# Kernel optimization log

Hardware: AMD Instinct MI355X
Metric: run time of the kernel (lower is better)

The kernel has to match this reference:

```python
import jax, jax.numpy as jnp
import numpy as np

N_TOKENS = 16384
MODEL_DIM = 2048
NUM_EXPERTS = 16
TOP_K = 2
CAPACITY_FACTOR = 1.0
NUM_SPLIT = 2  # os.environ 'num_split' default in source


def setup_inputs() -> dict:
    key = jax.random.key(0)
    kx, kw = jax.random.split(key)
    x = jax.random.normal(kx, (N_TOKENS, MODEL_DIM), dtype=jnp.float32)
    # kaiming_normal_ on Linear weight: std = sqrt(2 / fan_in)
    wg = jax.random.normal(kw, (NUM_EXPERTS, MODEL_DIM), dtype=jnp.float32) * np.float32(np.sqrt(2.0 / MODEL_DIM))
    return {"x": x, "wg": wg}


def _loss_compute(logits):
    gates = jax.nn.softmax(logits, axis=1)              # [N, E]
    num_experts = logits.shape[1]
    indices1_s = jnp.argmax(gates, axis=1)              # [N]
    mask1 = jax.nn.one_hot(indices1_s, num_experts, dtype=gates.dtype)
    me = jnp.mean(gates, axis=0)
    ce = jnp.mean(mask1, axis=0)
    l_aux = jnp.sum(me * ce) * num_experts
    return l_aux, indices1_s, gates


def _dispatch_fix_capacity(gates, k, capacity_factor, num_split):
    # gates is detached in the original (torch .detach())
    gates = jax.lax.stop_gradient(gates)
    n, e = gates.shape
    capacity = int(k * n // e * capacity_factor) // num_split * num_split
    values, topk_idx = jax.lax.top_k(gates, k)          # [N, k]
    weights = values
    flat_experts = topk_idx.reshape(-1)                 # [N*k]
    order = jnp.argsort(flat_experts)                   # stable sort by expert id
    experts_sorted = flat_experts[order]
    token_ids = jnp.repeat(jnp.arange(n, dtype=jnp.int32), k)[order]
    # position of each routed token within its expert's run
    counts = jax.ops.segment_sum(jnp.ones_like(flat_experts, dtype=jnp.int32), flat_experts, num_segments=e)
    starts = jnp.cumsum(counts) - counts                # exclusive prefix sum
    pos = jnp.arange(n * k, dtype=jnp.int32) - starts[experts_sorted]
    # fixed-capacity index table, -1 = empty slot; overflow tokens dropped
    ind = jnp.full((e, capacity), -1, dtype=jnp.int32)
    ind = ind.at[experts_sorted, pos].set(token_ids, mode="drop")  # pos>=capacity dropped
    indices = ind.reshape(-1)                           # [E*capacity], expert-major
    mask = indices >= 0
    expert_ids = jnp.repeat(jnp.arange(e, dtype=gates.dtype), capacity)
    return weights, indices, expert_ids, mask


def reference(x, wg):
    logits = jnp.einsum("nd,ed->ne", x, wg)             # Linear, no bias
    l_aux, _indices1, gates = _loss_compute(logits)
    weights, indices, expert_ids, mask = _dispatch_fix_capacity(
        gates, TOP_K, CAPACITY_FACTOR, NUM_SPLIT)
    return l_aux, weights, indices, expert_ids
```

## Files before the change

kernel.cpp:

```cpp
#include <hip/hip_runtime.h>
#include <hip/hip_bf16.h>
#include <stdint.h>

#define N_TOKENS    16384
#define MODEL_DIM   2048
#define NUM_EXPERTS 16
#define CAPACITY    2048
#define NBLK2       512
#define NBLK        256
#define GBLK        512
#define W_OFF       1
#define IDX_OFF     (1 + 2 * N_TOKENS)
#define EID_OFF     (IDX_OFF + NUM_EXPERTS * CAPACITY)

#define SC_E01    0
#define SC_CNTH   16384
#define SC_CEH    32768
#define SC_ME     49152

#define DPPX(v, ctrl) __int_as_float(__builtin_amdgcn_update_dpp(             \
    0, __float_as_int(v), (ctrl), 0xF, 0xF, true))
#define SWZ(v, off) __int_as_float(__builtin_amdgcn_ds_swizzle(               \
    __float_as_int(v), (off)))

__global__ __launch_bounds__(512) void k_logits(
    const float* __restrict__ x, const float* __restrict__ wg,
    float* __restrict__ out, uint8_t* __restrict__ ws)
{
  __shared__ float part[8][32][2][17];
  const int tid = threadIdx.x;
  const int b = blockIdx.x;
  const int l = tid & 63;
  const int kr = tid >> 6;
  const int kb = kr * 256 + l * 4;
  const int rot = l & 15;

  float4 w[16];
#pragma unroll
  for (int i = 0; i < NUM_EXPERTS; ++i)
    w[i] = *reinterpret_cast<const float4*>(wg + (size_t)((i ^ rot) * MODEL_DIM) + kb);

  const float* xp = x + (size_t)(b * 32) * MODEL_DIM + kb;

  float4 xc[4];
#pragma unroll
  for (int i = 0; i < 4; ++i)
    xc[i] = *reinterpret_cast<const float4*>(xp + (size_t)i * MODEL_DIM);

  for (int tb = 0; tb < 8; ++tb) {
    float4 xn[4];
    if (tb < 7) {
#pragma unroll
      for (int i = 0; i < 4; ++i)
        xn[i] = *reinterpret_cast<const float4*>(
            xp + (size_t)(tb * 4 + 4 + i) * MODEL_DIM);
    }
#pragma unroll
    for (int i = 0; i < 4; ++i) {
      const int t = tb * 4 + i;
      float cur[16];
#pragma unroll
      for (int j = 0; j < NUM_EXPERTS; ++j)
        cur[j] = xc[i].x * w[j].x + xc[i].y * w[j].y +
                 xc[i].z * w[j].z + xc[i].w * w[j].w;

#pragma unroll
      for (int r = 0; r < 8; ++r) cur[r] = cur[2 * r] + DPPX(cur[2 * r + 1], 0xB1);
#pragma unroll
      for (int r = 0; r < 4; ++r) cur[r] = cur[2 * r] + DPPX(cur[2 * r + 1], 0x4E);
#pragma unroll
      for (int r = 0; r < 2; ++r) cur[r] = cur[2 * r] + SWZ(cur[2 * r + 1], 0x101F);
      float v = cur[0] + DPPX(cur[1], 0x128);
      v += SWZ(v, 0x401F);
      if ((l & 31) < 16) part[kr][t][l >> 5][l & 15] = v;
    }
#pragma unroll
    for (int i = 0; i < 4; ++i) xc[i] = xn[i];
  }
  __syncthreads();

  if (tid < 32) {
    const int tg = b * 32 + tid;
    float logit[NUM_EXPERTS];
#pragma unroll
    for (int e4 = 0; e4 < 4; ++e4) {
      float4 s = *reinterpret_cast<const float4*>(&part[0][tid][0][e4 * 4]);
#pragma unroll
      for (int k2 = 0; k2 < 8; ++k2) {
#pragma unroll
        for (int h = 0; h < 2; ++h) {
          if (k2 == 0 && h == 0) continue;
          float4 p = *reinterpret_cast<const float4*>(&part[k2][tid][h][e4 * 4]);
          s.x += p.x; s.y += p.y; s.z += p.z; s.w += p.w;
        }
      }
      logit[e4 * 4 + 0] = s.x; logit[e4 * 4 + 1] = s.y;
      logit[e4 * 4 + 2] = s.z; logit[e4 * 4 + 3] = s.w;
    }

    float m = logit[0];
#pragma unroll
    for (int e = 1; e < NUM_EXPERTS; e++) m = fmaxf(m, logit[e]);
    float gg[NUM_EXPERTS]; float z = 0.f;
#pragma unroll
    for (int e = 0; e < NUM_EXPERTS; e++) { gg[e] = expf(logit[e] - m); z += gg[e]; }
    float inv = 1.f / z;
#pragma unroll
    for (int e = 0; e < NUM_EXPERTS; e++) gg[e] *= inv;

    float v1 = gg[0], v2 = -1.f; int e1 = 0, e2 = 0;
#pragma unroll
    for (int e = 1; e < NUM_EXPERTS; e++) {
      if (gg[e] > v1) { v2 = v1; e2 = e1; v1 = gg[e]; e1 = e; }
      else if (gg[e] > v2) { v2 = gg[e]; e2 = e; }
    }
    out[W_OFF + 2 * tg]     = v1;
    out[W_OFF + 2 * tg + 1] = v2;
    ws[SC_E01 + tg] = (uint8_t)(e1 | (e2 << 4));

    int mycount = 0, myce = 0;
    for (int e = 0; e < NUM_EXPERTS; e++) {
      unsigned long long m1 = __ballot(e1 == e);
      unsigned long long m2 = __ballot(e2 == e);
      if (tid == e) { mycount = __popcll(m1 | m2); myce = __popcll(m1); }
    }
    if (tid < NUM_EXPERTS) {
      reinterpret_cast<uint16_t*>(ws + SC_CNTH)[tid * NBLK2 + b] = (uint16_t)mycount;
      reinterpret_cast<uint16_t*>(ws + SC_CEH)[tid * NBLK2 + b] = (uint16_t)myce;
    }

#pragma unroll
    for (int e = 0; e < NUM_EXPERTS; e++) {
      gg[e] += __shfl_xor(gg[e], 1, 64);
      gg[e] += __shfl_xor(gg[e], 2, 64);
      gg[e] += __shfl_xor(gg[e], 4, 64);
      gg[e] += __shfl_xor(gg[e], 8, 64);
      gg[e] += __shfl_xor(gg[e], 16, 64);
    }
    if (tid == 0) {
      float* mp = reinterpret_cast<float*>(ws + SC_ME);
#pragma unroll
      for (int e = 0; e < NUM_EXPERTS; e++) mp[b * NUM_EXPERTS + e] = gg[e];
    }
  }
}

__global__ __launch_bounds__(192) void k_tail(
    const uint8_t* __restrict__ ws, float* __restrict__ out) {
  __shared__ int sstart[NUM_EXPERTS];
  __shared__ int stot[NUM_EXPERTS];
  const int tid = threadIdx.x;
  const int b = blockIdx.x;

  if (b == 256) {
    __shared__ float sme2[12][NUM_EXPERTS];
    __shared__ int sce2[12][NUM_EXPERTS];
    const float* me = reinterpret_cast<const float*>(ws + SC_ME);
    const uint16_t* ceh = reinterpret_cast<const uint16_t*>(ws + SC_CEH);
    const int e = tid & 15, grp = tid >> 4;
    float ms = 0.f; int cs = 0;
    for (int k = grp; k < NBLK2; k += 12) {
      ms += me[k * NUM_EXPERTS + e];
      cs += ceh[e * NBLK2 + k];
    }
    sme2[grp][e] = ms; sce2[grp][e] = cs;
    __syncthreads();
    if (tid < NUM_EXPERTS) {
      float ssum = 0.f; int ce = 0;
#pragma unroll
      for (int g2 = 0; g2 < 12; g2++) { ssum += sme2[g2][tid]; ce += sce2[g2][tid]; }
      float prod = (ssum * (1.0f / N_TOKENS)) * ((float)ce * (1.0f / N_TOKENS));
      prod += __shfl_xor(prod, 1, 64);
      prod += __shfl_xor(prod, 2, 64);
      prod += __shfl_xor(prod, 4, 64);
      prod += __shfl_xor(prod, 8, 64);
      if (tid == 0) out[0] = prod * (float)NUM_EXPERTS;
    }
    return;
  }

  if (tid < 64) {
    const int e = tid >> 2, q = tid & 3;
    const uint4* row =
        reinterpret_cast<const uint4*>(ws + SC_CNTH) + e * (NBLK2 / 8) + q * 16;
    const int limit = 2 * b;
    int s_lt = 0, s_all = 0;
    for (int wd = 0; wd < 16; ++wd) {
      uint4 v = row[wd];
      int p0 = (int)(v.x & 0xFFFF) + (int)(v.x >> 16);
      int p1 = (int)(v.y & 0xFFFF) + (int)(v.y >> 16);
      int p2 = (int)(v.z & 0xFFFF) + (int)(v.z >> 16);
      int p3 = (int)(v.w & 0xFFFF) + (int)(v.w >> 16);
      s_all += p0 + p1 + p2 + p3;
      const int base = q * 128 + wd * 8;
      if (base + 0 < limit) s_lt += p0;
      if (base + 2 < limit) s_lt += p1;
      if (base + 4 < limit) s_lt += p2;
      if (base + 6 < limit) s_lt += p3;
    }
    s_lt += __shfl_xor(s_lt, 1, 64);  s_lt += __shfl_xor(s_lt, 2, 64);
    s_all += __shfl_xor(s_all, 1, 64); s_all += __shfl_xor(s_all, 2, 64);
    if (q == 0) { sstart[e] = s_lt; stot[e] = s_all; }
  }
  __syncthreads();

  if (tid < 64) {
    const int t = b * 64 + tid;
    const int v = ws[SC_E01 + t];
    const int e1 = v & 15, e2 = v >> 4;
    const unsigned long long below = (1ull << tid) - 1ull;
    int p1 = CAPACITY, p2 = CAPACITY;
    for (int e = 0; e < NUM_EXPERTS; e++) {
      unsigned long long m = __ballot(e1 == e) | __ballot(e2 == e);
      int r = __popcll(m & below);
      int sbase = sstart[e];
      if (e1 == e) p1 = sbase + r;
      if (e2 == e) p2 = sbase + r;
    }
    float tf = (float)t;
    if ((unsigned)p1 < (unsigned)CAPACITY) out[IDX_OFF + e1 * CAPACITY + p1] = tf;
    if ((unsigned)p2 < (unsigned)CAPACITY) out[IDX_OFF + e2 * CAPACITY + p2] = tf;
  } else {
    const int slot = b * 128 + (tid - 64);
    const int e = slot >> 11;
    const int p = slot & (CAPACITY - 1);
    if (p >= stot[e]) out[IDX_OFF + slot] = -1.0f;
    out[EID_OFF + slot] = (float)e;
  }
}

extern "C" void kernel_launch(void* const* d_in, const int* in_sizes, int n_in,
                              void* d_out, int out_size, void* d_ws, size_t ws_size,
                              hipStream_t stream) {
  const float* x  = (const float*)d_in[0];
  const float* wg = (const float*)d_in[1];
  float* out = (float*)d_out;
  uint8_t* ws = (uint8_t*)d_ws;

  k_logits<<<GBLK, 512, 0, stream>>>(x, wg, out, ws);
  k_tail<<<257, 192, 0, stream>>>(ws, out);
}
```

Before: 52.08 us.

## Split logits reduction over 16 waves with float2 per-lane K slices

Doubles the k_logits block to 1024 threads, so each wave covers 128 K-elements using float2 loads instead of 256 with float4. The x prefetch becomes a two-row rolling buffer, and the LDS partial-sum array and the final cross-wave reduction grow to 16 slices. The aim is more waves in flight to hide memory latency and fewer registers per thread. In exchange, the per-token DPP/swizzle reduction work doubles relative to the FMAs, loads are narrower, and LDS use and the final reduction both grow.

```diff
diff --git a/kernel.cpp b/kernel.cpp
--- a/kernel.cpp
+++ b/kernel.cpp
@@ -23,59 +23,47 @@
 #define SWZ(v, off) __int_as_float(__builtin_amdgcn_ds_swizzle(               \
     __float_as_int(v), (off)))
 
-__global__ __launch_bounds__(512) void k_logits(
+__global__ __launch_bounds__(1024) void k_logits(
     const float* __restrict__ x, const float* __restrict__ wg,
     float* __restrict__ out, uint8_t* __restrict__ ws)
 {
-  __shared__ float part[8][32][2][17];
+  __shared__ float part[16][32][2][17];
   const int tid = threadIdx.x;
   const int b = blockIdx.x;
   const int l = tid & 63;
   const int kr = tid >> 6;
-  const int kb = kr * 256 + l * 4;
+  const int kb = kr * 128 + l * 2;
   const int rot = l & 15;
 
-  float4 w[16];
+  float2 w[16];
 #pragma unroll
   for (int i = 0; i < NUM_EXPERTS; ++i)
-    w[i] = *reinterpret_cast<const float4*>(wg + (size_t)((i ^ rot) * MODEL_DIM) + kb);
+    w[i] = *reinterpret_cast<const float2*>(wg + (size_t)((i ^ rot) * MODEL_DIM) + kb);
 
   const float* xp = x + (size_t)(b * 32) * MODEL_DIM + kb;
-
-  float4 xc[4];
-#pragma unroll
-  for (int i = 0; i < 4; ++i)
-    xc[i] = *reinterpret_cast<const float4*>(xp + (size_t)i * MODEL_DIM);
-
-  for (int tb = 0; tb < 8; ++tb) {
-    float4 xn[4];
-    if (tb < 7) {
-#pragma unroll
-      for (int i = 0; i < 4; ++i)
-        xn[i] = *reinterpret_cast<const float4*>(
-            xp + (size_t)(tb * 4 + 4 + i) * MODEL_DIM);
-    }
-#pragma unroll
-    for (int i = 0; i < 4; ++i) {
-      const int t = tb * 4 + i;
-      float cur[16];
-#pragma unroll
-      for (int j = 0; j < NUM_EXPERTS; ++j)
-        cur[j] = xc[i].x * w[j].x + xc[i].y * w[j].y +
-                 xc[i].z * w[j].z + xc[i].w * w[j].w;
-
-#pragma unroll
-      for (int r = 0; r < 8; ++r) cur[r] = cur[2 * r] + DPPX(cur[2 * r + 1], 0xB1);
-#pragma unroll
-      for (int r = 0; r < 4; ++r) cur[r] = cur[2 * r] + DPPX(cur[2 * r + 1], 0x4E);
-#pragma unroll
-      for (int r = 0; r < 2; ++r) cur[r] = cur[2 * r] + SWZ(cur[2 * r + 1], 0x101F);
-      float v = cur[0] + DPPX(cur[1], 0x128);
-      v += SWZ(v, 0x401F);
-      if ((l & 31) < 16) part[kr][t][l >> 5][l & 15] = v;
-    }
-#pragma unroll
-    for (int i = 0; i < 4; ++i) xc[i] = xn[i];
+  float2 xva = *reinterpret_cast<const float2*>(xp);
+  float2 xvb = *reinterpret_cast<const float2*>(xp + MODEL_DIM);
+
+  for (int t = 0; t < 32; ++t) {
+    float2 xvc;
+    if (t < 30)
+      xvc = *reinterpret_cast<const float2*>(xp + (size_t)(t + 2) * MODEL_DIM);
+
+    float cur[16];
+#pragma unroll
+    for (int i = 0; i < NUM_EXPERTS; ++i)
+      cur[i] = xva.x * w[i].x + xva.y * w[i].y;
+
+#pragma unroll
+    for (int r = 0; r < 8; ++r) cur[r] = cur[2 * r] + DPPX(cur[2 * r + 1], 0xB1);
+#pragma unroll
+    for (int r = 0; r < 4; ++r) cur[r] = cur[2 * r] + DPPX(cur[2 * r + 1], 0x4E);
+#pragma unroll
+    for (int r = 0; r < 2; ++r) cur[r] = cur[2 * r] + SWZ(cur[2 * r + 1], 0x101F);
+    float v = cur[0] + DPPX(cur[1], 0x128);
+    v += SWZ(v, 0x401F);
+    if ((l & 31) < 16) part[kr][t][l >> 5][l & 15] = v;
+    xva = xvb; xvb = xvc;
   }
   __syncthreads();
 
@@ -86,7 +74,7 @@
     for (int e4 = 0; e4 < 4; ++e4) {
       float4 s = *reinterpret_cast<const float4*>(&part[0][tid][0][e4 * 4]);
 #pragma unroll
-      for (int k2 = 0; k2 < 8; ++k2) {
+      for (int k2 = 0; k2 < 16; ++k2) {
 #pragma unroll
         for (int h = 0; h < 2; ++h) {
           if (k2 == 0 && h == 0) continue;
@@ -237,6 +225,6 @@
   float* out = (float*)d_out;
   uint8_t* ws = (uint8_t*)d_ws;
 
-  k_logits<<<GBLK, 512, 0, stream>>>(x, wg, out, ws);
+  k_logits<<<GBLK, 1024, 0, stream>>>(x, wg, out, ws);
   k_tail<<<257, 192, 0, stream>>>(ws, out);
 }
```

Result: slower. 56.12 us (+7.7%).

## Stream x rows through an LDS ring buffer via async global-to-LDS loads

Applied to the files above, without the earlier changes.

Replaces the register double-buffered x loads in the logits kernel with direct global_load_lds transfers into a 5-slot per-wavefront LDS ring. Each token step issues the load for the token four rows ahead, then waits with vmcnt(4) before reading the current slot. The aim is to keep more loads in flight and cut VGPR pressure, hiding HBM latency. The cost is extra LDS per block (40KB) and an LDS read per token. Occupancy may also drop, and the manual waitcnt ordering is fragile. The last iterations issue wrapped, redundant loads.

```diff
diff --git a/kernel.cpp b/kernel.cpp
--- a/kernel.cpp
+++ b/kernel.cpp
@@ -23,11 +23,17 @@
 #define SWZ(v, off) __int_as_float(__builtin_amdgcn_ds_swizzle(               \
     __float_as_int(v), (off)))
 
+#define ASYNC16(gsrc, ldst)                                                   \
+  __builtin_amdgcn_global_load_lds(                                           \
+      (const __attribute__((address_space(1))) void*)(gsrc),                  \
+      (__attribute__((address_space(3))) void*)(ldst), 16, 0, 0)
+
 __global__ __launch_bounds__(512) void k_logits(
     const float* __restrict__ x, const float* __restrict__ wg,
     float* __restrict__ out, uint8_t* __restrict__ ws)
 {
   __shared__ float part[8][32][2][17];
+  __shared__ float ring[8][5][256];
   const int tid = threadIdx.x;
   const int b = blockIdx.x;
   const int l = tid & 63;
@@ -42,41 +48,44 @@
 
   const float* xp = x + (size_t)(b * 32) * MODEL_DIM + kb;
 
-  float4 xc[4];
-#pragma unroll
-  for (int i = 0; i < 4; ++i)
-    xc[i] = *reinterpret_cast<const float4*>(xp + (size_t)i * MODEL_DIM);
-
-  for (int tb = 0; tb < 8; ++tb) {
-    float4 xn[4];
-    if (tb < 7) {
-#pragma unroll
-      for (int i = 0; i < 4; ++i)
-        xn[i] = *reinterpret_cast<const float4*>(
-            xp + (size_t)(tb * 4 + 4 + i) * MODEL_DIM);
-    }
-#pragma unroll
-    for (int i = 0; i < 4; ++i) {
-      const int t = tb * 4 + i;
-      float cur[16];
-#pragma unroll
-      for (int j = 0; j < NUM_EXPERTS; ++j)
-        cur[j] = xc[i].x * w[j].x + xc[i].y * w[j].y +
-                 xc[i].z * w[j].z + xc[i].w * w[j].w;
-
-#pragma unroll
-      for (int r = 0; r < 8; ++r) cur[r] = cur[2 * r] + DPPX(cur[2 * r + 1], 0xB1);
-#pragma unroll
-      for (int r = 0; r < 4; ++r) cur[r] = cur[2 * r] + DPPX(cur[2 * r + 1], 0x4E);
-#pragma unroll
-      for (int r = 0; r < 2; ++r) cur[r] = cur[2 * r] + SWZ(cur[2 * r + 1], 0x101F);
-      float v = cur[0] + DPPX(cur[1], 0x128);
-      v += SWZ(v, 0x401F);
-      if ((l & 31) < 16) part[kr][t][l >> 5][l & 15] = v;
-    }
-#pragma unroll
-    for (int i = 0; i < 4; ++i) xc[i] = xn[i];
-  }
+  ASYNC16(xp + (size_t)0 * MODEL_DIM, &ring[kr][0][0]);
+  ASYNC16(xp + (size_t)1 * MODEL_DIM, &ring[kr][1][0]);
+  ASYNC16(xp + (size_t)2 * MODEL_DIM, &ring[kr][2][0]);
+  ASYNC16(xp + (size_t)3 * MODEL_DIM, &ring[kr][3][0]);
+
+#define TOK_BODY(T, RS, WS)                                                    \
+  {                                                                            \
+    ASYNC16(xp + (size_t)(((T) + 4) & 31) * MODEL_DIM, &ring[kr][(WS)][0]);    \
+    asm volatile("s_waitcnt vmcnt(4)" ::: "memory");                           \
+    float4 xva = *reinterpret_cast<const float4*>(&ring[kr][(RS)][l * 4]);     \
+    float cur[16];                                                             \
+    _Pragma("unroll")                                                          \
+    for (int i = 0; i < NUM_EXPERTS; ++i)                                      \
+      cur[i] = xva.x * w[i].x + xva.y * w[i].y + xva.z * w[i].z +              \
+               xva.w * w[i].w;                                                 \
+    _Pragma("unroll")                                                          \
+    for (int r = 0; r < 8; ++r) cur[r] = cur[2 * r] + DPPX(cur[2 * r + 1], 0xB1); \
+    _Pragma("unroll")                                                          \
+    for (int r = 0; r < 4; ++r) cur[r] = cur[2 * r] + DPPX(cur[2 * r + 1], 0x4E); \
+    _Pragma("unroll")                                                          \
+    for (int r = 0; r < 2; ++r) cur[r] = cur[2 * r] + SWZ(cur[2 * r + 1], 0x101F); \
+    float vv = cur[0] + DPPX(cur[1], 0x128);                                   \
+    vv += SWZ(vv, 0x401F);                                                     \
+    if ((l & 31) < 16) part[kr][(T)][l >> 5][l & 15] = vv;                     \
+  }
+
+#pragma unroll 1
+  for (int u = 0; u < 6; ++u) {
+    const int t0 = u * 5;
+    TOK_BODY(t0 + 0, 0, 4)
+    TOK_BODY(t0 + 1, 1, 0)
+    TOK_BODY(t0 + 2, 2, 1)
+    TOK_BODY(t0 + 3, 3, 2)
+    TOK_BODY(t0 + 4, 4, 3)
+  }
+  TOK_BODY(30, 0, 4)
+  TOK_BODY(31, 1, 0)
+#undef TOK_BODY
   __syncthreads();
 
   if (tid < 32) {
```

Measured after the change: 51.99 us. About the same (-0.2%).
